# Kernel tuning notes

Hardware: AMD Instinct MI355X
Metric: run time of the kernel (lower is better)

## Reference

```python
import jax, jax.numpy as jnp
import numpy as np

N, T, V, F = 16, 128, 64, 16


def setup_inputs() -> dict:
    key = jax.random.key(0)
    k1, k2 = jax.random.split(key)
    x = jax.random.normal(k1, (N, T, V, F), dtype=jnp.float32)
    a_spatial = jax.random.normal(k2, (F, 1), dtype=jnp.float32) * 0.05
    return {"x": x, "a_spatial": a_spatial}


def reference(x, a_spatial):
    # x: [N, T, V, F]; pairwise abs-diff across vertices -> [N, T, V, V, F]
    diff = jnp.abs(x[:, :, :, None, :] - x[:, :, None, :, :])
    # mean over time -> [N, V, V, F] (matches transpose([0,4,2,3,1]) + reduce_mean(axis=1))
    mean_diff = jnp.mean(diff, axis=1)
    # score: dot with a_Spatial [F,1] then squeeze -> [N, V, V]
    score = jnp.einsum('nijf,fo->nij', mean_diff, a_spatial)
    tmpS = jnp.exp(jax.nn.relu(score))
    # row-normalize over axis=1 (as in the original K.sum(..., axis=1))
    return tmpS / jnp.sum(tmpS, axis=1, keepdims=True)
```

## Files before the change

### kernel.cpp

```cpp
#include <hip/hip_runtime.h>
#include <hip/hip_bf16.h>
#include <math.h>


#define Nn 16
#define Tt 128
#define Vv 64
#define Ff 16
#define CHUNKS 16
#define TC 8
#define JSPLIT 4
#define JPW 4

__global__ __launch_bounds__(256) void gls_scores(const float* __restrict__ x,
                                                  const float* __restrict__ a,
                                                  float* __restrict__ ws) {
    const int c   = blockIdx.x;
    const int n   = blockIdx.y;
    const int z   = blockIdx.z;
    const int tid = threadIdx.x;
    const int i   = tid & 63;
    const int w   = __builtin_amdgcn_readfirstlane(tid >> 6);
    const int j0  = z * (Vv / JSPLIT) + w * JPW;

    float af[Ff];
#pragma unroll
    for (int f = 0; f < Ff; ++f) af[f] = a[f];

    float acc[JPW] = {0.f, 0.f, 0.f, 0.f};

    const float* xnc = x + (size_t)(n * Tt + c * TC) * (Vv * Ff);

#pragma unroll 2
    for (int tt = 0; tt < TC; ++tt) {
        const float* xt = xnc + tt * (Vv * Ff);
        const float4 A0 = *(const float4*)(xt + i * Ff + 0);
        const float4 A1 = *(const float4*)(xt + i * Ff + 4);
        const float4 A2 = *(const float4*)(xt + i * Ff + 8);
        const float4 A3 = *(const float4*)(xt + i * Ff + 12);
#pragma unroll
        for (int jj = 0; jj < JPW; ++jj) {
            const float* xb = xt + (j0 + jj) * Ff;
            const float4 B0 = *(const float4*)(xb + 0);
            const float4 B1 = *(const float4*)(xb + 4);
            const float4 B2 = *(const float4*)(xb + 8);
            const float4 B3 = *(const float4*)(xb + 12);
            float s = acc[jj];
            s = fmaf(fabsf(A0.x - B0.x), af[0],  s);
            s = fmaf(fabsf(A0.y - B0.y), af[1],  s);
            s = fmaf(fabsf(A0.z - B0.z), af[2],  s);
            s = fmaf(fabsf(A0.w - B0.w), af[3],  s);
            s = fmaf(fabsf(A1.x - B1.x), af[4],  s);
            s = fmaf(fabsf(A1.y - B1.y), af[5],  s);
            s = fmaf(fabsf(A1.z - B1.z), af[6],  s);
            s = fmaf(fabsf(A1.w - B1.w), af[7],  s);
            s = fmaf(fabsf(A2.x - B2.x), af[8],  s);
            s = fmaf(fabsf(A2.y - B2.y), af[9],  s);
            s = fmaf(fabsf(A2.z - B2.z), af[10], s);
            s = fmaf(fabsf(A2.w - B2.w), af[11], s);
            s = fmaf(fabsf(A3.x - B3.x), af[12], s);
            s = fmaf(fabsf(A3.y - B3.y), af[13], s);
            s = fmaf(fabsf(A3.z - B3.z), af[14], s);
            s = fmaf(fabsf(A3.w - B3.w), af[15], s);
            acc[jj] = s;
        }
    }

    float* wsb = ws + (((size_t)n * CHUNKS + c) * Vv + j0) * Vv;
#pragma unroll
    for (int jj = 0; jj < JPW; ++jj)
        wsb[jj * Vv + i] = acc[jj];
}

__global__ __launch_bounds__(256) void gls_norm(const float* __restrict__ ws,
                                                float* __restrict__ out) {
    const int n   = blockIdx.x;
    const int jq  = blockIdx.y;
    const int tid = threadIdx.x;
    const int i   = tid & 63;
    const int w   = tid >> 6;
    const int j   = jq * 4 + w;

    const float* wsn = ws + (size_t)n * CHUNKS * (Vv * Vv);
    float s = 0.f;
#pragma unroll
    for (int cc = 0; cc < CHUNKS; ++cc)
        s += wsn[(cc * Vv + j) * Vv + i];

    const float e = expf(fmaxf(s * (1.0f / (float)Tt), 0.0f));
    float tsum = e;
#pragma unroll
    for (int m = 1; m < 64; m <<= 1) tsum += __shfl_xor(tsum, m, 64);

    out[((size_t)n * Vv + i) * Vv + j] = e / tsum;
}

extern "C" void kernel_launch(void* const* d_in, const int* in_sizes, int n_in,
                              void* d_out, int out_size, void* d_ws, size_t ws_size,
                              hipStream_t stream) {
    const float* x = (const float*)d_in[0];
    const float* a = (const float*)d_in[1];
    float* out = (float*)d_out;
    float* ws  = (float*)d_ws;

    dim3 g1(CHUNKS, Nn, JSPLIT);
    gls_scores<<<g1, 256, 0, stream>>>(x, a, ws);
    dim3 g2(Nn, 16);
    gls_norm<<<g2, 256, 0, stream>>>(ws, out);
}
```

Baseline: 70.29 us.

## Stage x time-chunk in padded shared memory and double chunk count

The scores kernel now loads each time chunk of x cooperatively into LDS with a padded pitch of 20 floats. The per-thread A and broadcast B rows are then read from shared memory instead of global memory. The time chunk is halved (TC 4, CHUNKS 32) to double the grid and shrink the LDS footprint, and launch bounds request 8 blocks per SM. The cost is a barrier per block, twice the partial-sum workspace, and twice the reduction work in the norm kernel.

```diff
diff --git a/kernel.cpp b/kernel.cpp
--- a/kernel.cpp
+++ b/kernel.cpp
@@ -7,14 +7,17 @@
 #define Tt 128
 #define Vv 64
 #define Ff 16
-#define CHUNKS 16
-#define TC 8
+#define CHUNKS 32
+#define TC 4
 #define JSPLIT 4
 #define JPW 4
+#define PITCH 20
 
-__global__ __launch_bounds__(256) void gls_scores(const float* __restrict__ x,
-                                                  const float* __restrict__ a,
-                                                  float* __restrict__ ws) {
+__global__ __launch_bounds__(256, 8) void gls_scores(const float* __restrict__ x,
+                                                     const float* __restrict__ a,
+                                                     float* __restrict__ ws) {
+    __shared__ float xs[TC * Vv * PITCH];
+
     const int c   = blockIdx.x;
     const int n   = blockIdx.y;
     const int z   = blockIdx.z;
@@ -23,28 +26,41 @@
     const int w   = __builtin_amdgcn_readfirstlane(tid >> 6);
     const int j0  = z * (Vv / JSPLIT) + w * JPW;
 
+    const float4* xg = (const float4*)(x + (size_t)(n * Tt + c * TC) * (Vv * Ff));
+#pragma unroll
+    for (int k = 0; k < 4; ++k) {
+        const int f4  = tid + k * 256;
+        const float4 val = xg[f4];
+        const int p   = f4 << 2;
+        const int tl  = p >> 10;
+        const int rem = p & 1023;
+        const int v   = rem >> 4;
+        const int f   = rem & 15;
+        *(float4*)&xs[(tl * Vv + v) * PITCH + f] = val;
+    }
+
     float af[Ff];
 #pragma unroll
     for (int f = 0; f < Ff; ++f) af[f] = a[f];
 
+    __syncthreads();
+
     float acc[JPW] = {0.f, 0.f, 0.f, 0.f};
 
-    const float* xnc = x + (size_t)(n * Tt + c * TC) * (Vv * Ff);
-
-#pragma unroll 2
+#pragma unroll
     for (int tt = 0; tt < TC; ++tt) {
-        const float* xt = xnc + tt * (Vv * Ff);
-        const float4 A0 = *(const float4*)(xt + i * Ff + 0);
-        const float4 A1 = *(const float4*)(xt + i * Ff + 4);
-        const float4 A2 = *(const float4*)(xt + i * Ff + 8);
-        const float4 A3 = *(const float4*)(xt + i * Ff + 12);
+        const float* xi = &xs[(tt * Vv + i) * PITCH];
+        const float4 A0 = *(const float4*)(xi);
+        const float4 A1 = *(const float4*)(xi + 4);
+        const float4 A2 = *(const float4*)(xi + 8);
+        const float4 A3 = *(const float4*)(xi + 12);
 #pragma unroll
         for (int jj = 0; jj < JPW; ++jj) {
-            const float* xb = xt + (j0 + jj) * Ff;
-            const float4 B0 = *(const float4*)(xb + 0);
-            const float4 B1 = *(const float4*)(xb + 4);
-            const float4 B2 = *(const float4*)(xb + 8);
-            const float4 B3 = *(const float4*)(xb + 12);
+            const float* xj = &xs[(tt * Vv + j0 + jj) * PITCH];
+            const float4 B0 = *(const float4*)(xj);
+            const float4 B1 = *(const float4*)(xj + 4);
+            const float4 B2 = *(const float4*)(xj + 8);
+            const float4 B3 = *(const float4*)(xj + 12);
             float s = acc[jj];
             s = fmaf(fabsf(A0.x - B0.x), af[0],  s);
             s = fmaf(fabsf(A0.y - B0.y), af[1],  s);
```

After: 70.04 us. Within noise of the previous version (-0.4%).
